# Kernel tuning notes

Measured on AMD Instinct MI355X. Metric: run time of the kernel, lower is better.

The kernel has to match this reference:

```python
import jax, jax.numpy as jnp
import numpy as np

H = 128
G = 8192            # num session graphs
TOTAL = 409600      # total nodes across all graphs
MAX_ITEM = 10000


def setup_inputs() -> dict:
    key = jax.random.key(0)
    ks = jax.random.split(key, 16)
    rng = np.random.default_rng(0)
    # variable-length sections that sum exactly to TOTAL
    secs = rng.integers(10, 90, size=G - 1)
    last = TOTAL - int(secs.sum())
    assert last >= 1
    sections = np.concatenate([secs, [last]]).astype(np.int32)
    segment_ids = np.repeat(np.arange(G, dtype=np.int32), sections)
    last_idx = (np.cumsum(sections) - 1).astype(np.int32)

    s = 0.02
    inp = {
        "node_embedding": jax.random.normal(ks[0], (TOTAL, H), jnp.float32),
        "num_count": jax.random.uniform(ks[1], (TOTAL,), jnp.float32),
        "sections": jnp.asarray(sections),
        "segment_ids": jnp.asarray(segment_ids),
        "last_idx": jnp.asarray(last_idx),
        "item_embedding_table": jax.random.normal(ks[2], (MAX_ITEM, H), jnp.float32),
        "user_embedding": jax.random.normal(ks[3], (G, H), jnp.float32),
        "u_n_repeat": jnp.zeros((G, H), jnp.float32),
        "max_item_id": MAX_ITEM,
        "W1_w": jax.random.normal(ks[4], (H, H), jnp.float32) * s,
        "W1_b": jnp.zeros((H,), jnp.float32),
        "W2_w": jax.random.normal(ks[5], (H, H), jnp.float32) * s,
        "W2_b": jnp.zeros((H,), jnp.float32),
        "q_w": jax.random.normal(ks[6], (1, H), jnp.float32) * s,
        "q_b": jnp.zeros((1,), jnp.float32),
        "W3_w": jax.random.normal(ks[7], (H, 2 * H), jnp.float32) * s,
        "W3_b": jnp.zeros((H,), jnp.float32),
    }
    return inp


def reference(node_embedding, num_count, sections, segment_ids, last_idx,
              item_embedding_table, user_embedding, u_n_repeat, max_item_id,
              W1_w, W1_b, W2_w, W2_b, q_w, q_b, W3_w, W3_b):
    num_graphs = last_idx.shape[0]
    # last node of each graph, [G, H]
    v_n = node_embedding[last_idx]
    # broadcast last node back to every node of its graph (replaces torch.split repeat loop)
    v_n_rep = v_n[segment_ids]                          # [N, H]
    gate = jax.nn.sigmoid(v_n_rep @ W1_w.T + W1_b + node_embedding @ W2_w.T + W2_b)
    alpha = gate @ q_w.T + q_b                          # [N, 1]
    s_g_whole = num_count[:, None] * alpha * node_embedding  # [N, H]
    s_g = jax.ops.segment_sum(s_g_whole, segment_ids, num_segments=num_graphs)  # [G, H]
    s_h = jnp.concatenate([v_n, s_g], axis=1) @ W3_w.T + W3_b  # [G, H]
    return s_h
```

## Files before the change

### kernel.cpp

```cpp
#include <hip/hip_runtime.h>
#include <hip/hip_bf16.h>

#define H_DIM  128
#define NGRAPH 8192
#define NTOTAL 409600

typedef __attribute__((ext_vector_type(8))) short    s16x8;
typedef __attribute__((ext_vector_type(4))) float    f32x4;
typedef __attribute__((ext_vector_type(4))) unsigned u32x4;

__device__ __forceinline__ unsigned short f2bf(float f) {
    unsigned int u = __float_as_uint(f);
    unsigned int r = u + 0x7fffu + ((u >> 16) & 1u);
    return (unsigned short)(r >> 16);
}

__global__ void k0_w2(const float* __restrict__ W2w, unsigned short* __restrict__ w2bf) {
    int i = blockIdx.x * 256 + threadIdx.x;
    w2bf[i] = f2bf(W2w[i]);
}

__global__ __launch_bounds__(128) void k1_ag(
    const float* __restrict__ node_emb,
    const int*   __restrict__ last_idx,
    const float* __restrict__ W1w,
    const float* __restrict__ W1b,
    const float* __restrict__ W2b,
    float* __restrict__ a_g,
    float* __restrict__ s_g)
{
    __shared__ float vn[4][H_DIM];
    const int tid = threadIdx.x;
    const int g0  = blockIdx.x * 4;
    #pragma unroll
    for (int g = 0; g < 4; g++) {
        int li = last_idx[g0 + g];
        vn[g][tid] = node_emb[(size_t)li * H_DIM + tid];
        s_g[(size_t)(g0 + g) * H_DIM + tid] = 0.f;
    }
    __syncthreads();
    float b = W1b[tid] + W2b[tid];
    float a0 = b, a1 = b, a2 = b, a3 = b;
    const float* wrow = W1w + (size_t)tid * H_DIM;
    #pragma unroll 8
    for (int k = 0; k < H_DIM; k += 4) {
        float4 w = *reinterpret_cast<const float4*>(wrow + k);
        a0 += w.x * vn[0][k] + w.y * vn[0][k+1] + w.z * vn[0][k+2] + w.w * vn[0][k+3];
        a1 += w.x * vn[1][k] + w.y * vn[1][k+1] + w.z * vn[1][k+2] + w.w * vn[1][k+3];
        a2 += w.x * vn[2][k] + w.y * vn[2][k+1] + w.z * vn[2][k+2] + w.w * vn[2][k+3];
        a3 += w.x * vn[3][k] + w.y * vn[3][k+1] + w.z * vn[3][k+2] + w.w * vn[3][k+3];
    }
    a_g[(size_t)(g0 + 0) * H_DIM + tid] = a0;
    a_g[(size_t)(g0 + 1) * H_DIM + tid] = a1;
    a_g[(size_t)(g0 + 2) * H_DIM + tid] = a2;
    a_g[(size_t)(g0 + 3) * H_DIM + tid] = a3;
}

__global__ __launch_bounds__(256, 4) void k2_fused(
    const float* __restrict__ node_emb,
    const float* __restrict__ num_count,
    const int*   __restrict__ seg_ids,
    const float* __restrict__ a_g,
    const unsigned short* __restrict__ w2bf,
    const float* __restrict__ q_w,
    const float* __restrict__ q_b,
    float* __restrict__ s_g)
{
    __shared__ __align__(16) char w2s[H_DIM * 256];

    const int tid = threadIdx.x;
    {
        const uint4* wsrc = reinterpret_cast<const uint4*>(w2bf);
        #pragma unroll
        for (int i = 0; i < 8; i++) {
            int c = i * 256 + tid;
            uint4 v = wsrc[c];
            int byte = c << 4;
            int row  = byte >> 8;
            *reinterpret_cast<uint4*>(w2s + (byte ^ ((row & 7) << 4))) = v;
        }
    }

    const int lane = tid & 63;
    const int wid  = tid >> 6;
    const int l16 = lane & 15, lq = lane >> 4;
    const int nb  = (blockIdx.x * 4 + wid) * 16;

    const int   sgl = seg_ids[nb + l16];
    const float ncl = num_count[nb + l16];
    const float qb0 = q_b[0];

    s16x8 af[4];
    const float* nrow = node_emb + (size_t)(nb + l16) * H_DIM + lq * 8;
    #pragma unroll
    for (int ks = 0; ks < 4; ks++) {
        float4 f0 = *reinterpret_cast<const float4*>(nrow + ks * 32);
        float4 f1 = *reinterpret_cast<const float4*>(nrow + ks * 32 + 4);
        unsigned p0, p1, p2, p3;
        asm("v_cvt_pk_bf16_f32 %0, %1, %2" : "=v"(p0) : "v"(f0.x), "v"(f0.y));
        asm("v_cvt_pk_bf16_f32 %0, %1, %2" : "=v"(p1) : "v"(f0.z), "v"(f0.w));
        asm("v_cvt_pk_bf16_f32 %0, %1, %2" : "=v"(p2) : "v"(f1.x), "v"(f1.y));
        asm("v_cvt_pk_bf16_f32 %0, %1, %2" : "=v"(p3) : "v"(f1.z), "v"(f1.w));
        union { u32x4 u; s16x8 s; } cv;
        cv.u = u32x4{p0, p1, p2, p3};
        af[ks] = cv.s;
    }

    __syncthreads();

    f32x4 acc[8];
    #pragma unroll
    for (int nt = 0; nt < 8; nt++) acc[nt] = f32x4{0.f, 0.f, 0.f, 0.f};
    #pragma unroll
    for (int ks = 0; ks < 4; ks++) {
        #pragma unroll
        for (int nt = 0; nt < 8; nt++) {
            int row  = nt * 16 + l16;
            int byte = (row << 8) | ((lq * 8 + ks * 32) << 1);
            byte ^= (row & 7) << 4;
            s16x8 wfr = *reinterpret_cast<const s16x8*>(w2s + byte);
            acc[nt] = __builtin_amdgcn_mfma_f32_16x16x32_bf16(wfr, af[ks], acc[nt], 0, 0, 0);
        }
    }
    __builtin_amdgcn_sched_barrier(0);

    const float* agrow = a_g + (size_t)sgl * H_DIM + lq * 4;
    float p = 0.f;
    #pragma unroll
    for (int nt = 0; nt < 8; nt++) {
        float4 q4 = *reinterpret_cast<const float4*>(q_w + nt * 16 + lq * 4);
        float4 a4 = *reinterpret_cast<const float4*>(agrow + nt * 16);
        float zq[4] = {a4.x, a4.y, a4.z, a4.w};
        float qq[4] = {q4.x, q4.y, q4.z, q4.w};
        #pragma unroll
        for (int rr = 0; rr < 4; rr++) {
            float z = acc[nt][rr] + zq[rr];
            float e = __expf(-z);
            p += qq[rr] * __builtin_amdgcn_rcpf(1.f + e);
        }
    }
    p += __shfl_xor(p, 16, 64);
    p += __shfl_xor(p, 32, 64);
    const float coefl = ncl * (p + qb0);

    s16x8 ib[2];
    #pragma unroll
    for (int b = 0; b < 2; b++) {
        int kk = l16 + 16 * b;
        #pragma unroll
        for (int e = 0; e < 8; e++)
            ib[b][e] = (kk == lq * 8 + e) ? (short)0x3F80 : (short)0;
    }
    f32x4 accT[4][2];
    #pragma unroll
    for (int ks = 0; ks < 4; ks++)
        #pragma unroll
        for (int b = 0; b < 2; b++)
            accT[ks][b] = __builtin_amdgcn_mfma_f32_16x16x32_bf16(
                              af[ks], ib[b], f32x4{0.f, 0.f, 0.f, 0.f}, 0, 0, 0);

    int r0 = 0;
    while (r0 < 16) {
        const int cur = __shfl(sgl, r0, 64);
        unsigned long long diff = __ballot(sgl != cur) & 0xFFFFull;
        diff &= ~((1ull << r0) - 1ull);
        const int r1 = diff ? (int)__builtin_ctzll(diff) : 16;

        const float cmask = (sgl == cur) ? coefl : 0.f;
        float cm[4];
        #pragma unroll
        for (int rr = 0; rr < 4; rr++)
            cm[rr] = __shfl(cmask, lq * 4 + rr, 64);

        #pragma unroll
        for (int ks = 0; ks < 4; ks++) {
            #pragma unroll
            for (int b = 0; b < 2; b++) {
                float s = cm[0] * accT[ks][b][0] + cm[1] * accT[ks][b][1]
                        + cm[2] * accT[ks][b][2] + cm[3] * accT[ks][b][3];
                s += __shfl_xor(s, 16, 64);
                s += __shfl_xor(s, 32, 64);
                if (lq == 0)
                    atomicAdd(s_g + (size_t)cur * H_DIM + ks * 32 + b * 16 + l16, s);
            }
        }
        r0 = r1;
    }
}

__global__ __launch_bounds__(128) void k3_out(
    const float* __restrict__ node_emb,
    const int*   __restrict__ last_idx,
    const float* __restrict__ s_g,
    const float* __restrict__ W3w,
    const float* __restrict__ W3b,
    float* __restrict__ out)
{
    __shared__ float cat[8][2 * H_DIM];
    const int tid = threadIdx.x;
    const int g0  = blockIdx.x * 8;
    #pragma unroll
    for (int g = 0; g < 8; g++) {
        cat[g][tid]         = node_emb[(size_t)last_idx[g0 + g] * H_DIM + tid];
        cat[g][H_DIM + tid] = s_g[(size_t)(g0 + g) * H_DIM + tid];
    }
    __syncthreads();
    float acc[8];
    float b = W3b[tid];
    #pragma unroll
    for (int g = 0; g < 8; g++) acc[g] = b;
    const float* wrow = W3w + (size_t)tid * (2 * H_DIM);
    for (int k = 0; k < 2 * H_DIM; k += 4) {
        float4 w = *reinterpret_cast<const float4*>(wrow + k);
        #pragma unroll
        for (int g = 0; g < 8; g++)
            acc[g] += w.x * cat[g][k] + w.y * cat[g][k+1]
                    + w.z * cat[g][k+2] + w.w * cat[g][k+3];
    }
    #pragma unroll
    for (int g = 0; g < 8; g++)
        out[(size_t)(g0 + g) * H_DIM + tid] = acc[g];
}

extern "C" void kernel_launch(void* const* d_in, const int* in_sizes, int n_in,
                              void* d_out, int out_size, void* d_ws, size_t ws_size,
                              hipStream_t stream) {
    const float* node_emb  = (const float*)d_in[0];
    const float* num_count = (const float*)d_in[1];
    const int*   seg_ids   = (const int*)d_in[3];
    const int*   last_idx  = (const int*)d_in[4];
    const float* W1w = (const float*)d_in[9];
    const float* W1b = (const float*)d_in[10];
    const float* W2w = (const float*)d_in[11];
    const float* W2b = (const float*)d_in[12];
    const float* qw  = (const float*)d_in[13];
    const float* qb  = (const float*)d_in[14];
    const float* W3w = (const float*)d_in[15];
    const float* W3b = (const float*)d_in[16];
    float* out = (float*)d_out;

    char* ws = (char*)d_ws;
    float* a_g = (float*)(ws);
    float* s_g = (float*)(ws + (4u << 20));
    unsigned short* w2bf = (unsigned short*)(ws + (8u << 20));

    k0_w2   <<<64,          256, 0, stream>>>(W2w, w2bf);
    k1_ag   <<<NGRAPH / 4,  128, 0, stream>>>(node_emb, last_idx, W1w, W1b, W2b, a_g, s_g);
    k2_fused<<<NTOTAL / 64, 256, 0, stream>>>(node_emb, num_count, seg_ids, a_g,
                                              w2bf, qw, qb, s_g);
    k3_out  <<<NGRAPH / 8,  128, 0, stream>>>(node_emb, last_idx, s_g, W3w, W3b, out);
}
```

Before: 109.1 us.

## Make k2 persistent with double-buffered global-to-LDS node prefetch

The main kernel becomes persistent: 256 blocks of 6 waves each walk a contiguous range of 16-node jobs. Each job prefetches the next tile of node embeddings straight into LDS with global_load_lds and double-buffers it. The W2 bf16 tile is loaded into shared memory once per block rather than once per 64 nodes, and a_g is folded into the MFMA accumulator's initial value. The aim is to amortise the W2 staging and hide global load latency. In exchange, occupancy drops because of the larger LDS footprint (96KB node buffers plus 32KB W2), and each wave runs its jobs serially behind a full vmcnt(0) wait.

```diff
diff --git a/kernel.cpp b/kernel.cpp
--- a/kernel.cpp
+++ b/kernel.cpp
@@ -4,6 +4,10 @@
 #define H_DIM  128
 #define NGRAPH 8192
 #define NTOTAL 409600
+#define NJOBS  (NTOTAL / 16)
+#define NBLK   256
+#define WPB    6
+#define NWAVES (NBLK * WPB)
 
 typedef __attribute__((ext_vector_type(8))) short    s16x8;
 typedef __attribute__((ext_vector_type(4))) float    f32x4;
@@ -13,6 +17,13 @@
     unsigned int u = __float_as_uint(f);
     unsigned int r = u + 0x7fffu + ((u >> 16) & 1u);
     return (unsigned short)(r >> 16);
+}
+
+__device__ __forceinline__ void gload_lds16(const void* g, void* l) {
+    __builtin_amdgcn_global_load_lds(
+        (const __attribute__((address_space(1))) unsigned int*)g,
+        (__attribute__((address_space(3))) unsigned int*)l,
+        16, 0, 0);
 }
 
 __global__ void k0_w2(const float* __restrict__ W2w, unsigned short* __restrict__ w2bf) {
@@ -56,7 +67,7 @@
     a_g[(size_t)(g0 + 3) * H_DIM + tid] = a3;
 }
 
-__global__ __launch_bounds__(256, 4) void k2_fused(
+__global__ __launch_bounds__(384, 2) void k2_fused(
     const float* __restrict__ node_emb,
     const float* __restrict__ num_count,
     const int*   __restrict__ seg_ids,
@@ -66,83 +77,37 @@
     const float* __restrict__ q_b,
     float* __restrict__ s_g)
 {
+    __shared__ __align__(16) char ndbuf[WPB][2][8192];
     __shared__ __align__(16) char w2s[H_DIM * 256];
 
     const int tid = threadIdx.x;
     {
         const uint4* wsrc = reinterpret_cast<const uint4*>(w2bf);
         #pragma unroll
-        for (int i = 0; i < 8; i++) {
-            int c = i * 256 + tid;
-            uint4 v = wsrc[c];
-            int byte = c << 4;
-            int row  = byte >> 8;
-            *reinterpret_cast<uint4*>(w2s + (byte ^ ((row & 7) << 4))) = v;
+        for (int i = 0; i < 6; i++) {
+            int c = i * 384 + tid;
+            if (c < 2048) {
+                uint4 v = wsrc[c];
+                int byte = c << 4;
+                int row  = byte >> 8;
+                *reinterpret_cast<uint4*>(w2s + (byte ^ ((row & 7) << 4))) = v;
+            }
         }
     }
 
     const int lane = tid & 63;
     const int wid  = tid >> 6;
     const int l16 = lane & 15, lq = lane >> 4;
-    const int nb  = (blockIdx.x * 4 + wid) * 16;
-
-    const int   sgl = seg_ids[nb + l16];
-    const float ncl = num_count[nb + l16];
-    const float qb0 = q_b[0];
-
-    s16x8 af[4];
-    const float* nrow = node_emb + (size_t)(nb + l16) * H_DIM + lq * 8;
-    #pragma unroll
-    for (int ks = 0; ks < 4; ks++) {
-        float4 f0 = *reinterpret_cast<const float4*>(nrow + ks * 32);
-        float4 f1 = *reinterpret_cast<const float4*>(nrow + ks * 32 + 4);
-        unsigned p0, p1, p2, p3;
-        asm("v_cvt_pk_bf16_f32 %0, %1, %2" : "=v"(p0) : "v"(f0.x), "v"(f0.y));
-        asm("v_cvt_pk_bf16_f32 %0, %1, %2" : "=v"(p1) : "v"(f0.z), "v"(f0.w));
-        asm("v_cvt_pk_bf16_f32 %0, %1, %2" : "=v"(p2) : "v"(f1.x), "v"(f1.y));
-        asm("v_cvt_pk_bf16_f32 %0, %1, %2" : "=v"(p3) : "v"(f1.z), "v"(f1.w));
-        union { u32x4 u; s16x8 s; } cv;
-        cv.u = u32x4{p0, p1, p2, p3};
-        af[ks] = cv.s;
-    }
-
-    __syncthreads();
-
-    f32x4 acc[8];
-    #pragma unroll
-    for (int nt = 0; nt < 8; nt++) acc[nt] = f32x4{0.f, 0.f, 0.f, 0.f};
-    #pragma unroll
-    for (int ks = 0; ks < 4; ks++) {
-        #pragma unroll
-        for (int nt = 0; nt < 8; nt++) {
-            int row  = nt * 16 + l16;
-            int byte = (row << 8) | ((lq * 8 + ks * 32) << 1);
-            byte ^= (row & 7) << 4;
-            s16x8 wfr = *reinterpret_cast<const s16x8*>(w2s + byte);
-            acc[nt] = __builtin_amdgcn_mfma_f32_16x16x32_bf16(wfr, af[ks], acc[nt], 0, 0, 0);
-        }
-    }
-    __builtin_amdgcn_sched_barrier(0);
-
-    const float* agrow = a_g + (size_t)sgl * H_DIM + lq * 4;
-    float p = 0.f;
+    const int gw = blockIdx.x * WPB + wid;
+    const int j0 = (int)(((long)gw       * NJOBS) / NWAVES);
+    const int j1 = (int)(((long)(gw + 1) * NJOBS) / NWAVES);
+
+    float qv[8][4];
     #pragma unroll
     for (int nt = 0; nt < 8; nt++) {
         float4 q4 = *reinterpret_cast<const float4*>(q_w + nt * 16 + lq * 4);
-        float4 a4 = *reinterpret_cast<const float4*>(agrow + nt * 16);
-        float zq[4] = {a4.x, a4.y, a4.z, a4.w};
-        float qq[4] = {q4.x, q4.y, q4.z, q4.w};
-        #pragma unroll
-        for (int rr = 0; rr < 4; rr++) {
-            float z = acc[nt][rr] + zq[rr];
-            float e = __expf(-z);
-            p += qq[rr] * __builtin_amdgcn_rcpf(1.f + e);
-        }
-    }
-    p += __shfl_xor(p, 16, 64);
-    p += __shfl_xor(p, 32, 64);
-    const float coefl = ncl * (p + qb0);
-
+        qv[nt][0] = q4.x; qv[nt][1] = q4.y; qv[nt][2] = q4.z; qv[nt][3] = q4.w;
+    }
     s16x8 ib[2];
     #pragma unroll
     for (int b = 0; b < 2; b++) {
@@ -151,40 +116,133 @@
         for (int e = 0; e < 8; e++)
             ib[b][e] = (kk == lq * 8 + e) ? (short)0x3F80 : (short)0;
     }
-    f32x4 accT[4][2];
-    #pragma unroll
-    for (int ks = 0; ks < 4; ks++)
-        #pragma unroll
-        for (int b = 0; b < 2; b++)
-            accT[ks][b] = __builtin_amdgcn_mfma_f32_16x16x32_bf16(
-                              af[ks], ib[b], f32x4{0.f, 0.f, 0.f, 0.f}, 0, 0, 0);
-
-    int r0 = 0;
-    while (r0 < 16) {
-        const int cur = __shfl(sgl, r0, 64);
-        unsigned long long diff = __ballot(sgl != cur) & 0xFFFFull;
-        diff &= ~((1ull << r0) - 1ull);
-        const int r1 = diff ? (int)__builtin_ctzll(diff) : 16;
-
-        const float cmask = (sgl == cur) ? coefl : 0.f;
-        float cm[4];
-        #pragma unroll
-        for (int rr = 0; rr < 4; rr++)
-            cm[rr] = __shfl(cmask, lq * 4 + rr, 64);
-
+    const float qb0 = q_b[0];
+
+    char* bufA = &ndbuf[wid][0][0];
+    char* bufB = &ndbuf[wid][1][0];
+
+    {
+        const char* gbase = (const char*)node_emb + (size_t)j0 * 16 * 512;
+        #pragma unroll
+        for (int i = 0; i < 8; i++) {
+            int lin = i * 1024 + lane * 16;
+            int src = lin ^ (((lin >> 9) & 7) << 4);
+            gload_lds16(gbase + src, bufA + i * 1024);
+        }
+    }
+    int   sgN = seg_ids[j0 * 16 + l16];
+    float ncN = num_count[j0 * 16 + l16];
+
+    __syncthreads();
+
+    #pragma unroll 1
+    for (int j = j0; j < j1; j++) {
+        asm volatile("s_waitcnt vmcnt(0)" ::: "memory");
+        __builtin_amdgcn_sched_barrier(0);
+
+        const int   sgl = sgN;
+        const float ncl = ncN;
+
+        const float* agrow = a_g + (size_t)sgl * H_DIM + lq * 4;
+        float4 ag4[8];
+        #pragma unroll
+        for (int nt = 0; nt < 8; nt++)
+            ag4[nt] = *reinterpret_cast<const float4*>(agrow + nt * 16);
+
+        s16x8 af[4];
         #pragma unroll
         for (int ks = 0; ks < 4; ks++) {
-            #pragma unroll
-            for (int b = 0; b < 2; b++) {
-                float s = cm[0] * accT[ks][b][0] + cm[1] * accT[ks][b][1]
-                        + cm[2] * accT[ks][b][2] + cm[3] * accT[ks][b][3];
-                s += __shfl_xor(s, 16, 64);
-                s += __shfl_xor(s, 32, 64);
-                if (lq == 0)
-                    atomicAdd(s_g + (size_t)cur * H_DIM + ks * 32 + b * 16 + l16, s);
+            int base = l16 * 512 + lq * 32 + ks * 128;
+            float4 f0 = *reinterpret_cast<const float4*>(bufA + ( base        ^ ((l16 & 7) << 4)));
+            float4 f1 = *reinterpret_cast<const float4*>(bufA + ((base + 16) ^ ((l16 & 7) << 4)));
+            unsigned p0, p1, p2, p3;
+            asm("v_cvt_pk_bf16_f32 %0, %1, %2" : "=v"(p0) : "v"(f0.x), "v"(f0.y));
+            asm("v_cvt_pk_bf16_f32 %0, %1, %2" : "=v"(p1) : "v"(f0.z), "v"(f0.w));
+            asm("v_cvt_pk_bf16_f32 %0, %1, %2" : "=v"(p2) : "v"(f1.x), "v"(f1.y));
+            asm("v_cvt_pk_bf16_f32 %0, %1, %2" : "=v"(p3) : "v"(f1.z), "v"(f1.w));
+            union { u32x4 u; s16x8 s; } cv;
+            cv.u = u32x4{p0, p1, p2, p3};
+            af[ks] = cv.s;
+        }
+
+        if (j + 1 < j1) {
+            const char* gbase = (const char*)node_emb + (size_t)(j + 1) * 16 * 512;
+            #pragma unroll
+            for (int i = 0; i < 8; i++) {
+                int lin = i * 1024 + lane * 16;
+                int src = lin ^ (((lin >> 9) & 7) << 4);
+                gload_lds16(gbase + src, bufB + i * 1024);
             }
-        }
-        r0 = r1;
+            sgN = seg_ids[(j + 1) * 16 + l16];
+            ncN = num_count[(j + 1) * 16 + l16];
+        }
+
+        f32x4 acc[8];
+        #pragma unroll
+        for (int nt = 0; nt < 8; nt++)
+            acc[nt] = f32x4{ag4[nt].x, ag4[nt].y, ag4[nt].z, ag4[nt].w};
+        #pragma unroll
+        for (int ks = 0; ks < 4; ks++) {
+            #pragma unroll
+            for (int nt = 0; nt < 8; nt++) {
+                int row  = nt * 16 + l16;
+                int byte = (row << 8) | ((lq * 8 + ks * 32) << 1);
+                byte ^= (row & 7) << 4;
+                s16x8 wfr = *reinterpret_cast<const s16x8*>(w2s + byte);
+                acc[nt] = __builtin_amdgcn_mfma_f32_16x16x32_bf16(wfr, af[ks], acc[nt], 0, 0, 0);
+            }
+        }
+
+        float pp0 = 0.f, pp1 = 0.f, pp2 = 0.f, pp3 = 0.f;
+        #pragma unroll
+        for (int nt = 0; nt < 8; nt++) {
+            pp0 += qv[nt][0] * __builtin_amdgcn_rcpf(1.f + __expf(-acc[nt][0]));
+            pp1 += qv[nt][1] * __builtin_amdgcn_rcpf(1.f + __expf(-acc[nt][1]));
+            pp2 += qv[nt][2] * __builtin_amdgcn_rcpf(1.f + __expf(-acc[nt][2]));
+            pp3 += qv[nt][3] * __builtin_amdgcn_rcpf(1.f + __expf(-acc[nt][3]));
+        }
+        float p = (pp0 + pp1) + (pp2 + pp3);
+        p += __shfl_xor(p, 16, 64);
+        p += __shfl_xor(p, 32, 64);
+        const float coefl = ncl * (p + qb0);
+
+        f32x4 accT[4][2];
+        #pragma unroll
+        for (int ks = 0; ks < 4; ks++)
+            #pragma unroll
+            for (int b = 0; b < 2; b++)
+                accT[ks][b] = __builtin_amdgcn_mfma_f32_16x16x32_bf16(
+                                  af[ks], ib[b], f32x4{0.f, 0.f, 0.f, 0.f}, 0, 0, 0);
+
+        int r0 = 0;
+        while (r0 < 16) {
+            const int cur = __shfl(sgl, r0, 64);
+            unsigned long long diff = __ballot(sgl != cur) & 0xFFFFull;
+            diff &= ~((1ull << r0) - 1ull);
+            const int r1 = diff ? (int)__builtin_ctzll(diff) : 16;
+
+            const float cmask = (sgl == cur) ? coefl : 0.f;
+            float cm[4];
+            #pragma unroll
+            for (int rr = 0; rr < 4; rr++)
+                cm[rr] = __shfl(cmask, lq * 4 + rr, 64);
+
+            #pragma unroll
+            for (int ks = 0; ks < 4; ks++) {
+                #pragma unroll
+                for (int b = 0; b < 2; b++) {
+                    float s = cm[0] * accT[ks][b][0] + cm[1] * accT[ks][b][1]
+                            + cm[2] * accT[ks][b][2] + cm[3] * accT[ks][b][3];
+                    s += __shfl_xor(s, 16, 64);
+                    s += __shfl_xor(s, 32, 64);
+                    if (lq == 0)
+                        atomicAdd(s_g + (size_t)cur * H_DIM + ks * 32 + b * 16 + l16, s);
+                }
+            }
+            r0 = r1;
+        }
+
+        char* t = bufA; bufA = bufB; bufB = t;
     }
 }
 
@@ -244,9 +302,9 @@
     float* s_g = (float*)(ws + (4u << 20));
     unsigned short* w2bf = (unsigned short*)(ws + (8u << 20));
 
-    k0_w2   <<<64,          256, 0, stream>>>(W2w, w2bf);
-    k1_ag   <<<NGRAPH / 4,  128, 0, stream>>>(node_emb, last_idx, W1w, W1b, W2b, a_g, s_g);
-    k2_fused<<<NTOTAL / 64, 256, 0, stream>>>(node_emb, num_count, seg_ids, a_g,
-                                              w2bf, qw, qb, s_g);
-    k3_out  <<<NGRAPH / 8,  128, 0, stream>>>(node_emb, last_idx, s_g, W3w, W3b, out);
-}
+    k0_w2   <<<64,         256, 0, stream>>>(W2w, w2bf);
+    k1_ag   <<<NGRAPH / 4, 128, 0, stream>>>(node_emb, last_idx, W1w, W1b, W2b, a_g, s_g);
+    k2_fused<<<NBLK,       384, 0, stream>>>(node_emb, num_count, seg_ids, a_g,
+                                             w2bf, qw, qb, s_g);
+    k3_out  <<<NGRAPH / 8, 128, 0, stream>>>(node_emb, last_idx, s_g, W3w, W3b, out);
+}
```

Result: no change. 110.3 us (+1.1%).

## Fold -log2e into weights, seed MFMA accumulators with a_g, enlarge k2 blocks

Applied to the files above, without the earlier changes.

Pre-scales W2 and a_g by -log2(e) so the sigmoid becomes a bare exp2 plus rcp, and seeds the MFMA accumulators with the gathered a_g row instead of adding it afterwards. The k2 block grows to 512 threads (8 waves, 128 nodes), which halves the per-block LDS fill of W2, and the block index is remapped across the grid. Four independent partial sums replace the serial reduction chain. The a_g gather is now issued before the MFMAs, which overlaps its latency but holds more registers across the matmul.

```diff
diff --git a/kernel.cpp b/kernel.cpp
--- a/kernel.cpp
+++ b/kernel.cpp
@@ -4,6 +4,9 @@
 #define H_DIM  128
 #define NGRAPH 8192
 #define NTOTAL 409600
+#define NBLK2  (NTOTAL / 128)
+
+#define NLOG2E -1.4426950408889634f
 
 typedef __attribute__((ext_vector_type(8))) short    s16x8;
 typedef __attribute__((ext_vector_type(4))) float    f32x4;
@@ -17,7 +20,7 @@
 
 __global__ void k0_w2(const float* __restrict__ W2w, unsigned short* __restrict__ w2bf) {
     int i = blockIdx.x * 256 + threadIdx.x;
-    w2bf[i] = f2bf(W2w[i]);
+    w2bf[i] = f2bf(NLOG2E * W2w[i]);
 }
 
 __global__ __launch_bounds__(128) void k1_ag(
@@ -50,13 +53,13 @@
         a2 += w.x * vn[2][k] + w.y * vn[2][k+1] + w.z * vn[2][k+2] + w.w * vn[2][k+3];
         a3 += w.x * vn[3][k] + w.y * vn[3][k+1] + w.z * vn[3][k+2] + w.w * vn[3][k+3];
     }
-    a_g[(size_t)(g0 + 0) * H_DIM + tid] = a0;
-    a_g[(size_t)(g0 + 1) * H_DIM + tid] = a1;
-    a_g[(size_t)(g0 + 2) * H_DIM + tid] = a2;
-    a_g[(size_t)(g0 + 3) * H_DIM + tid] = a3;
-}
-
-__global__ __launch_bounds__(256, 4) void k2_fused(
+    a_g[(size_t)(g0 + 0) * H_DIM + tid] = NLOG2E * a0;
+    a_g[(size_t)(g0 + 1) * H_DIM + tid] = NLOG2E * a1;
+    a_g[(size_t)(g0 + 2) * H_DIM + tid] = NLOG2E * a2;
+    a_g[(size_t)(g0 + 3) * H_DIM + tid] = NLOG2E * a3;
+}
+
+__global__ __launch_bounds__(512, 6) void k2_fused(
     const float* __restrict__ node_emb,
     const float* __restrict__ num_count,
     const int*   __restrict__ seg_ids,
@@ -72,8 +75,8 @@
     {
         const uint4* wsrc = reinterpret_cast<const uint4*>(w2bf);
         #pragma unroll
-        for (int i = 0; i < 8; i++) {
-            int c = i * 256 + tid;
+        for (int i = 0; i < 4; i++) {
+            int c = i * 512 + tid;
             uint4 v = wsrc[c];
             int byte = c << 4;
             int row  = byte >> 8;
@@ -81,14 +84,25 @@
         }
     }
 
+    const int bid = (int)blockIdx.x;
+    const int swz = (bid & 7) * (NBLK2 / 8) + (bid >> 3);
+
     const int lane = tid & 63;
     const int wid  = tid >> 6;
     const int l16 = lane & 15, lq = lane >> 4;
-    const int nb  = (blockIdx.x * 4 + wid) * 16;
+    const int nb  = (swz * 8 + wid) * 16;
 
     const int   sgl = seg_ids[nb + l16];
     const float ncl = num_count[nb + l16];
     const float qb0 = q_b[0];
+
+    const float* agrow = a_g + (size_t)sgl * H_DIM + lq * 4;
+    f32x4 acc[8];
+    #pragma unroll
+    for (int nt = 0; nt < 8; nt++) {
+        float4 a4 = *reinterpret_cast<const float4*>(agrow + nt * 16);
+        acc[nt] = f32x4{a4.x, a4.y, a4.z, a4.w};
+    }
 
     s16x8 af[4];
     const float* nrow = node_emb + (size_t)(nb + l16) * H_DIM + lq * 8;
@@ -108,9 +122,6 @@
 
     __syncthreads();
 
-    f32x4 acc[8];
-    #pragma unroll
-    for (int nt = 0; nt < 8; nt++) acc[nt] = f32x4{0.f, 0.f, 0.f, 0.f};
     #pragma unroll
     for (int ks = 0; ks < 4; ks++) {
         #pragma unroll
@@ -122,23 +133,17 @@
             acc[nt] = __builtin_amdgcn_mfma_f32_16x16x32_bf16(wfr, af[ks], acc[nt], 0, 0, 0);
         }
     }
-    __builtin_amdgcn_sched_barrier(0);
-
-    const float* agrow = a_g + (size_t)sgl * H_DIM + lq * 4;
-    float p = 0.f;
+
+    float pp0 = 0.f, pp1 = 0.f, pp2 = 0.f, pp3 = 0.f;
     #pragma unroll
     for (int nt = 0; nt < 8; nt++) {
         float4 q4 = *reinterpret_cast<const float4*>(q_w + nt * 16 + lq * 4);
-        float4 a4 = *reinterpret_cast<const float4*>(agrow + nt * 16);
-        float zq[4] = {a4.x, a4.y, a4.z, a4.w};
-        float qq[4] = {q4.x, q4.y, q4.z, q4.w};
-        #pragma unroll
-        for (int rr = 0; rr < 4; rr++) {
-            float z = acc[nt][rr] + zq[rr];
-            float e = __expf(-z);
-            p += qq[rr] * __builtin_amdgcn_rcpf(1.f + e);
-        }
-    }
+        pp0 += q4.x * __builtin_amdgcn_rcpf(1.f + __builtin_amdgcn_exp2f(acc[nt][0]));
+        pp1 += q4.y * __builtin_amdgcn_rcpf(1.f + __builtin_amdgcn_exp2f(acc[nt][1]));
+        pp2 += q4.z * __builtin_amdgcn_rcpf(1.f + __builtin_amdgcn_exp2f(acc[nt][2]));
+        pp3 += q4.w * __builtin_amdgcn_rcpf(1.f + __builtin_amdgcn_exp2f(acc[nt][3]));
+    }
+    float p = (pp0 + pp1) + (pp2 + pp3);
     p += __shfl_xor(p, 16, 64);
     p += __shfl_xor(p, 32, 64);
     const float coefl = ncl * (p + qb0);
@@ -244,9 +249,9 @@
     float* s_g = (float*)(ws + (4u << 20));
     unsigned short* w2bf = (unsigned short*)(ws + (8u << 20));
 
-    k0_w2   <<<64,          256, 0, stream>>>(W2w, w2bf);
-    k1_ag   <<<NGRAPH / 4,  128, 0, stream>>>(node_emb, last_idx, W1w, W1b, W2b, a_g, s_g);
-    k2_fused<<<NTOTAL / 64, 256, 0, stream>>>(node_emb, num_count, seg_ids, a_g,
-                                              w2bf, qw, qb, s_g);
-    k3_out  <<<NGRAPH / 8,  128, 0, stream>>>(node_emb, last_idx, s_g, W3w, W3b, out);
-}
+    k0_w2   <<<64,         256, 0, stream>>>(W2w, w2bf);
+    k1_ag   <<<NGRAPH / 4, 128, 0, stream>>>(node_emb, last_idx, W1w, W1b, W2b, a_g, s_g);
+    k2_fused<<<NBLK2,      512, 0, stream>>>(node_emb, num_count, seg_ids, a_g,
+                                             w2bf, qw, qb, s_g);
+    k3_out  <<<NGRAPH / 8, 128, 0, stream>>>(node_emb, last_idx, s_g, W3w, W3b, out);
+}
```

Measured after the change: 107.2 us. Within noise of the previous version (-1.8%).
